# Kernel tuning notes

Measured on AMD Instinct MI355X. Metric: run time of the kernel, lower is better.

## Reference

```python
import jax, jax.numpy as jnp
import numpy as np

N, D, C = 4096, 2048, 8192
NUM_IDS = 256
MARGIN = 0.3
LABEL_SMOOTHING = 0.1


def setup_inputs() -> dict:
    key = jax.random.key(0)
    k1, k2, k3 = jax.random.split(key, 3)
    embeddings = jax.random.normal(k1, (N, D), dtype=jnp.float32)
    pred_ids = jax.random.normal(k2, (N, C), dtype=jnp.float32)
    target_ids = jax.random.randint(k3, (N,), 0, NUM_IDS, dtype=jnp.int64)
    return {"embeddings": embeddings, "pred_ids": pred_ids, "target_ids": target_ids}


def _euclidean_dist(x, y):
    xx = jnp.sum(x * x, axis=1, keepdims=True)            # [N,1]
    yy = jnp.sum(y * y, axis=1, keepdims=True).T          # [1,N]
    d2 = xx + yy - 2.0 * (x @ y.T)
    return jnp.sqrt(jnp.maximum(d2, 1e-12))


def _cross_entropy_ls(logits, targets, eps):
    # label-smoothed CE, mean over batch
    logp = jax.nn.log_softmax(logits, axis=-1)
    n_cls = logits.shape[-1]
    nll = -jnp.take_along_axis(logp, targets[:, None], axis=1)[:, 0]
    smooth = -jnp.mean(logp, axis=-1)
    return jnp.mean((1.0 - eps) * nll + eps * smooth)


def reference(embeddings, pred_ids, target_ids):
    # ID loss: cross entropy with label smoothing
    id_loss = _cross_entropy_ls(pred_ids, target_ids, LABEL_SMOOTHING)

    # Triplet loss with batch-hard mining
    dist = _euclidean_dist(embeddings, embeddings)        # [N,N]
    pos_mask = target_ids[:, None] == target_ids[None, :] # includes diagonal (as in original)
    neg_inf = jnp.float32(-jnp.inf)
    pos_inf = jnp.float32(jnp.inf)
    dist_ap = jnp.max(jnp.where(pos_mask, dist, neg_inf), axis=1)  # hardest positive
    dist_an = jnp.min(jnp.where(pos_mask, pos_inf, dist), axis=1)  # hardest negative

    # MarginRankingLoss with y=1: mean(relu(dist_ap - dist_an + margin))
    tri_loss = jnp.mean(jnp.maximum(dist_ap - dist_an + MARGIN, 0.0))

    return (id_loss, tri_loss, dist_ap, dist_an)
```

## Files before the change

### kernel.cpp

```cpp
#include <hip/hip_runtime.h>
#include <hip/hip_bf16.h>

typedef unsigned short u16;
typedef unsigned int u32;
typedef __attribute__((ext_vector_type(8))) __bf16 bf16x8;
typedef __attribute__((ext_vector_type(4))) float f32x4;

#define NROW 4096
#define DDIM 2048
#define NCLS 8192
#define MARGIN 0.3f
#define EPS_LS 0.1f
#define FLT_MAX_ 3.402823466e+38f

#define GLOBAL_AS __attribute__((address_space(1)))
#define LDS_AS __attribute__((address_space(3)))

__device__ __forceinline__ void gload_lds16(const void* g, void* l) {
    __builtin_amdgcn_global_load_lds((const GLOBAL_AS u32*)g, (LDS_AS u32*)l, 16, 0, 0);
}

__device__ __forceinline__ u16 f2bf(float f) {
    u32 b = __float_as_uint(f);
    u32 r = (b + 0x7FFFu + ((b >> 16) & 1u)) >> 16;
    return (u16)r;
}

__global__ __launch_bounds__(256) void prep_kernel(
    const float* __restrict__ emb, u16* __restrict__ e16,
    float* __restrict__ xx, int* __restrict__ ap, int* __restrict__ an)
{
    int row = blockIdx.x, tid = threadIdx.x;
    const float4* p = (const float4*)(emb + (size_t)row * DDIM);
    float4 a = p[tid * 2], b = p[tid * 2 + 1];
    float s = a.x*a.x + a.y*a.y + a.z*a.z + a.w*a.w
            + b.x*b.x + b.y*b.y + b.z*b.z + b.w*b.w;

    uint4 pk;
    pk.x = (u32)f2bf(a.x) | ((u32)f2bf(a.y) << 16);
    pk.y = (u32)f2bf(a.z) | ((u32)f2bf(a.w) << 16);
    pk.z = (u32)f2bf(b.x) | ((u32)f2bf(b.y) << 16);
    pk.w = (u32)f2bf(b.z) | ((u32)f2bf(b.w) << 16);
    *(uint4*)&e16[(size_t)row * DDIM + tid * 8] = pk;

    #pragma unroll
    for (int o = 1; o < 64; o <<= 1) s += __shfl_xor(s, o);
    __shared__ float sred[4];
    if ((tid & 63) == 0) sred[tid >> 6] = s;
    __syncthreads();
    if (tid == 0) {
        xx[row] = sred[0] + sred[1] + sred[2] + sred[3];
        ap[row] = 0x80000000;
        an[row] = 0x7FFFFFFF;
    }
}

__global__ __launch_bounds__(256) void ce_kernel(
    const float* __restrict__ pred, const int* __restrict__ tgt,
    float* __restrict__ out)
{
    int row = blockIdx.x, tid = threadIdx.x;
    const float4* p = (const float4*)(pred + (size_t)row * NCLS);
    float4 v[8];
    #pragma unroll
    for (int i = 0; i < 8; ++i) v[i] = p[tid + i * 256];

    float mx = -FLT_MAX_, sm = 0.f;
    #pragma unroll
    for (int i = 0; i < 8; ++i) {
        mx = fmaxf(mx, fmaxf(fmaxf(v[i].x, v[i].y), fmaxf(v[i].z, v[i].w)));
        sm += v[i].x + v[i].y + v[i].z + v[i].w;
    }
    #pragma unroll
    for (int o = 1; o < 64; o <<= 1) {
        mx = fmaxf(mx, __shfl_xor(mx, o));
        sm += __shfl_xor(sm, o);
    }
    __shared__ float smx[4], ssm[4], sse[4];
    int w = tid >> 6;
    if ((tid & 63) == 0) { smx[w] = mx; ssm[w] = sm; }
    __syncthreads();
    mx = fmaxf(fmaxf(smx[0], smx[1]), fmaxf(smx[2], smx[3]));
    sm = ssm[0] + ssm[1] + ssm[2] + ssm[3];

    float es = 0.f;
    #pragma unroll
    for (int i = 0; i < 8; ++i) {
        es += expf(v[i].x - mx) + expf(v[i].y - mx)
            + expf(v[i].z - mx) + expf(v[i].w - mx);
    }
    #pragma unroll
    for (int o = 1; o < 64; o <<= 1) es += __shfl_xor(es, o);
    if ((tid & 63) == 0) sse[w] = es;
    __syncthreads();
    if (tid == 0) {
        es = sse[0] + sse[1] + sse[2] + sse[3];
        float lse = mx + logf(es);
        int t = tgt[row];
        float lt = pred[(size_t)row * NCLS + t];
        float loss = (1.0f - EPS_LS) * (lse - lt)
                   + EPS_LS * (lse - sm * (1.0f / NCLS));
        atomicAdd(out, loss * (1.0f / NROW));
    }
}

__global__ __launch_bounds__(256) void gram_kernel(
    const u16* __restrict__ e16, const float* __restrict__ xx,
    const int* __restrict__ tg, int* __restrict__ ap, int* __restrict__ an)
{
    __shared__ __align__(16) u16 lsA[128 * 64];
    __shared__ __align__(16) u16 lsB[128 * 64];

    int bid = blockIdx.x;
    int wg  = ((bid & 7) << 7) | (bid >> 3);
    int tm  = wg >> 5, tn = wg & 31;
    int rowBase = tm * 128, colBase = tn * 128;

    int tid = threadIdx.x;
    int wid = tid >> 6, lane = tid & 63;
    int wm = wid >> 1, wn = wid & 1;

    f32x4 acc[4][4];
    #pragma unroll
    for (int i = 0; i < 4; ++i)
        #pragma unroll
        for (int j = 0; j < 4; ++j) acc[i][j] = (f32x4){0.f, 0.f, 0.f, 0.f};

    int srow = lane >> 3;
    int sslot = lane & 7;

    for (int kb = 0; kb < DDIM; kb += 64) {
        #pragma unroll
        for (int t = 0; t < 4; ++t) {
            int r0 = (wid * 4 + t) * 8;
            int r  = r0 + srow;
            int gsl = sslot ^ (r & 7);
            const u16* ga = &e16[(size_t)(rowBase + r) * DDIM + kb + gsl * 8];
            gload_lds16(ga, &lsA[r0 * 64]);
            const u16* gb = &e16[(size_t)(colBase + r) * DDIM + kb + gsl * 8];
            gload_lds16(gb, &lsB[r0 * 64]);
        }
        __syncthreads();

        #pragma unroll
        for (int h = 0; h < 2; ++h) {
            bf16x8 af[4], bfr[4];
            #pragma unroll
            for (int fm = 0; fm < 4; ++fm) {
                int row = wm * 64 + fm * 16 + (lane & 15);
                int sl = (h * 4 + (lane >> 4)) ^ (row & 7);
                af[fm] = *(const bf16x8*)&lsA[row * 64 + sl * 8];
            }
            #pragma unroll
            for (int fn = 0; fn < 4; ++fn) {
                int row = wn * 64 + fn * 16 + (lane & 15);
                int sl = (h * 4 + (lane >> 4)) ^ (row & 7);
                bfr[fn] = *(const bf16x8*)&lsB[row * 64 + sl * 8];
            }
            #pragma unroll
            for (int fm = 0; fm < 4; ++fm)
                #pragma unroll
                for (int fn = 0; fn < 4; ++fn)
                    acc[fm][fn] = __builtin_amdgcn_mfma_f32_16x16x32_bf16(
                        af[fm], bfr[fn], acc[fm][fn], 0, 0, 0);
        }
        __syncthreads();
    }

    float xc[4]; int tc[4];
    #pragma unroll
    for (int fn = 0; fn < 4; ++fn) {
        int gc = colBase + wn * 64 + fn * 16 + (lane & 15);
        xc[fn] = xx[gc];
        tc[fn] = tg[gc];
    }
    #pragma unroll
    for (int fm = 0; fm < 4; ++fm) {
        #pragma unroll
        for (int reg = 0; reg < 4; ++reg) {
            int gr = rowBase + wm * 64 + fm * 16 + (lane >> 4) * 4 + reg;
            float xr = xx[gr];
            int   tr = tg[gr];
            float cap = -FLT_MAX_, can = FLT_MAX_;
            #pragma unroll
            for (int fn = 0; fn < 4; ++fn) {
                int gc = colBase + wn * 64 + fn * 16 + (lane & 15);
                float d2 = xr + xc[fn] - 2.0f * acc[fm][fn][reg];
                d2 = fmaxf(d2, 0.0f);
                if (gr == gc) d2 = 0.0f;
                if (tr == tc[fn]) cap = fmaxf(cap, d2);
                else              can = fminf(can, d2);
            }
            #pragma unroll
            for (int o = 1; o < 16; o <<= 1) {
                cap = fmaxf(cap, __shfl_xor(cap, o));
                can = fminf(can, __shfl_xor(can, o));
            }
            if ((lane & 15) == 0) {
                atomicMax(&ap[gr], __float_as_int(cap));
                atomicMin(&an[gr], __float_as_int(can));
            }
        }
    }
}

__global__ __launch_bounds__(256) void final_kernel(
    const int* __restrict__ ap, const int* __restrict__ an,
    float* __restrict__ out)
{
    int i = blockIdx.x * 256 + threadIdx.x;
    float a2 = __int_as_float(ap[i]);
    float n2 = __int_as_float(an[i]);
    float av = sqrtf(fmaxf(a2, 1e-12f));
    float nv = sqrtf(fmaxf(n2, 1e-12f));
    out[2 + i] = av;
    out[2 + NROW + i] = nv;
    float t = fmaxf(av - nv + MARGIN, 0.0f);
    #pragma unroll
    for (int o = 1; o < 64; o <<= 1) t += __shfl_xor(t, o);
    __shared__ float sred[4];
    if ((threadIdx.x & 63) == 0) sred[threadIdx.x >> 6] = t;
    __syncthreads();
    if (threadIdx.x == 0)
        atomicAdd(out + 1, (sred[0] + sred[1] + sred[2] + sred[3]) * (1.0f / NROW));
}

extern "C" void kernel_launch(void* const* d_in, const int* in_sizes, int n_in,
                              void* d_out, int out_size, void* d_ws, size_t ws_size,
                              hipStream_t stream)
{
    const float* emb  = (const float*)d_in[0];
    const float* pred = (const float*)d_in[1];
    const int*   tgt  = (const int*)d_in[2];
    float* out = (float*)d_out;

    char* ws = (char*)d_ws;
    u16*   e16 = (u16*)ws;
    float* xx  = (float*)(ws + (size_t)16 * 1024 * 1024);
    int*   ap  = (int*)(ws + (size_t)16 * 1024 * 1024 + 16384);
    int*   an  = (int*)(ws + (size_t)16 * 1024 * 1024 + 32768);

    hipMemsetAsync(d_out, 0, 2 * sizeof(float), stream);
    prep_kernel <<<NROW, 256, 0, stream>>>(emb, e16, xx, ap, an);
    ce_kernel   <<<NROW, 256, 0, stream>>>(pred, tgt, out);
    gram_kernel <<<1024, 256, 0, stream>>>(e16, xx, tgt, ap, an);
    final_kernel<<<NROW / 256, 256, 0, stream>>>(ap, an, out);
}
```

Measured before the change: 337.5 us.

## Exploit Gram symmetry: compute upper-triangular tiles and reduce both rows and columns

The Gram kernel now launches only the 528 upper-triangular 128x128 tiles instead of all 1024. Each block maps its linear index to (tm, tn) through a sqrt-based triangular inverse with correction loops. Off-diagonal tiles also reduce per-column hardest positive and negative distances and update those rows with atomics, so the mirrored tile does not need computing. This roughly halves the MFMA and load work, at the cost of extra epilogue reductions and column atomics. It also leaves fewer blocks, which may underfill the GPU's CUs.

```diff
diff --git a/kernel.cpp b/kernel.cpp
--- a/kernel.cpp
+++ b/kernel.cpp
@@ -112,9 +112,14 @@
     __shared__ __align__(16) u16 lsB[128 * 64];
 
     int bid = blockIdx.x;
-    int wg  = ((bid & 7) << 7) | (bid >> 3);
-    int tm  = wg >> 5, tn = wg & 31;
+    int wg  = (bid & 7) * 66 + (bid >> 3);
+    int tm = (int)(32.5f - sqrtf(32.5f * 32.5f - 2.0f * (float)wg));
+    if (tm < 0) tm = 0;
+    while (tm < 31 && (tm + 1) * (65 - (tm + 1)) / 2 <= wg) ++tm;
+    while (tm > 0 && tm * (65 - tm) / 2 > wg) --tm;
+    int tn = tm + (wg - tm * (65 - tm) / 2);
     int rowBase = tm * 128, colBase = tn * 128;
+    bool diag = (tm == tn);
 
     int tid = threadIdx.x;
     int wid = tid >> 6, lane = tid & 63;
@@ -168,11 +173,14 @@
     }
 
     float xc[4]; int tc[4];
+    float capc[4], canc[4];
     #pragma unroll
     for (int fn = 0; fn < 4; ++fn) {
         int gc = colBase + wn * 64 + fn * 16 + (lane & 15);
         xc[fn] = xx[gc];
         tc[fn] = tg[gc];
+        capc[fn] = -FLT_MAX_;
+        canc[fn] = FLT_MAX_;
     }
     #pragma unroll
     for (int fm = 0; fm < 4; ++fm) {
@@ -188,8 +196,9 @@
                 float d2 = xr + xc[fn] - 2.0f * acc[fm][fn][reg];
                 d2 = fmaxf(d2, 0.0f);
                 if (gr == gc) d2 = 0.0f;
-                if (tr == tc[fn]) cap = fmaxf(cap, d2);
-                else              can = fminf(can, d2);
+                bool pos = (tr == tc[fn]);
+                if (pos) { cap = fmaxf(cap, d2); capc[fn] = fmaxf(capc[fn], d2); }
+                else     { can = fminf(can, d2); canc[fn] = fminf(canc[fn], d2); }
             }
             #pragma unroll
             for (int o = 1; o < 16; o <<= 1) {
@@ -199,6 +208,21 @@
             if ((lane & 15) == 0) {
                 atomicMax(&ap[gr], __float_as_int(cap));
                 atomicMin(&an[gr], __float_as_int(can));
+            }
+        }
+    }
+    if (!diag) {
+        #pragma unroll
+        for (int fn = 0; fn < 4; ++fn) {
+            float cap = capc[fn], can = canc[fn];
+            cap = fmaxf(cap, __shfl_xor(cap, 16));
+            can = fminf(can, __shfl_xor(can, 16));
+            cap = fmaxf(cap, __shfl_xor(cap, 32));
+            can = fminf(can, __shfl_xor(can, 32));
+            if (lane < 16) {
+                int gc = colBase + wn * 64 + fn * 16 + lane;
+                atomicMax(&ap[gc], __float_as_int(cap));
+                atomicMin(&an[gc], __float_as_int(can));
             }
         }
     }
@@ -243,6 +267,6 @@
     hipMemsetAsync(d_out, 0, 2 * sizeof(float), stream);
     prep_kernel <<<NROW, 256, 0, stream>>>(emb, e16, xx, ap, an);
     ce_kernel   <<<NROW, 256, 0, stream>>>(pred, tgt, out);
-    gram_kernel <<<1024, 256, 0, stream>>>(e16, xx, tgt, ap, an);
+    gram_kernel <<<528, 256, 0, stream>>>(e16, xx, tgt, ap, an);
     final_kernel<<<NROW / 256, 256, 0, stream>>>(ap, an, out);
 }
```

New measurement: 330.4 us. -2.1%, faster.
